# Kernel tuning notes

Hardware: AMD Instinct MI355X
Metric: run time of the kernel (lower is better)

## Reference

```python
import jax, jax.numpy as jnp
import numpy as np

N = 100000   # nodes
E = 400000   # edges
IN = 256
OUT = 256
R = 200      # num relations
B = 32       # num bases


def setup_inputs() -> dict:
    key = jax.random.key(0)
    ks = jax.random.split(key, 7)
    in_feat = jax.random.normal(ks[0], (N, IN), jnp.float32)
    src = jax.random.randint(ks[1], (E,), 0, N, dtype=jnp.int32)
    dst = jax.random.randint(ks[2], (E,), 0, N, dtype=jnp.int32)
    etype = jax.random.randint(ks[3], (E,), 0, R, dtype=jnp.int32)
    # learned params (xavier-ish scale)
    basis = jax.random.normal(ks[4], (B, IN * OUT), jnp.float32) * 0.01
    coef = jax.random.normal(ks[5], (R, B), jnp.float32) * 0.1
    self_loop_weight = jax.random.normal(ks[6], (IN, OUT), jnp.float32) * 0.05
    return {"in_feat": in_feat, "basis": basis, "coef": coef,
            "self_loop_weight": self_loop_weight,
            "src": src, "dst": dst, "etype": etype}


def _rgcn_forward(in_feat, basis, coef, self_loop_weight, src, dst, etype):
    # W_r = reshape(coef @ basis) -> [R, IN, OUT]; msg_e = h_src[e] @ W[etype[e]].
    # Equivalently msg_e = sum_b coef[etype[e], b] * (h_src[e] @ basis_b),
    # computed as B large GEMMs (scan over bases) instead of E tiny bmms,
    # avoiding the [E, IN, OUT] per-edge weight gather.
    basis3 = basis.reshape(B, IN, OUT)          # [B, IN, OUT]
    src_h = in_feat[src]                        # [E, IN]
    c = coef[etype]                             # [E, B]

    def body(acc, xs):
        w_b, c_b = xs                           # [IN, OUT], [E]
        return acc + (src_h @ w_b) * c_b[:, None], None

    msg0 = jnp.zeros((E, OUT), in_feat.dtype)
    msg, _ = jax.lax.scan(body, msg0, (basis3, c.T))   # [E, OUT]

    # mean aggregation over destination nodes (dgl fn.mean)
    agg = jax.ops.segment_sum(msg, dst, num_segments=N)            # [N, OUT]
    deg = jax.ops.segment_sum(jnp.ones((E,), in_feat.dtype), dst, num_segments=N)
    out = agg / jnp.maximum(deg, 1.0)[:, None]  # zero-in-degree nodes -> 0

    # self-loop (bias=False, activation=None, dropout eval no-op)
    out = out + in_feat @ self_loop_weight
    return out


def reference(in_feat, basis, coef, self_loop_weight, src, dst, etype):
    return _rgcn_forward(in_feat, basis, coef, self_loop_weight, src, dst, etype)
```

## Files before the change

### kernel.cpp

```cpp
#include <hip/hip_runtime.h>
#include <hip/hip_bf16.h>


#define NN 100000
#define EE 400000
#define RR 200
#define BB 32
#define MAXTILES 6464
#define EQ2 (MAXTILES * 2 / 8)
#define SCHUNK 2048
#define NSCAN ((NN + 255) / 256)

typedef __attribute__((ext_vector_type(8))) short short8v;
typedef __attribute__((ext_vector_type(4))) float f32x4;

__device__ __forceinline__ unsigned short f2bf(float f) {
  unsigned u = __float_as_uint(f);
  u += 0x7FFF + ((u >> 16) & 1);
  return (unsigned short)(u >> 16);
}
__device__ __forceinline__ float bf2f(unsigned short h) {
  return __uint_as_float(((unsigned)h) << 16);
}

template <bool FEAT>
__global__ __launch_bounds__(256) void k_prep1(
    const float* __restrict__ basis, const float* __restrict__ coef,
    const float* __restrict__ slw, const int* __restrict__ etype,
    const int* __restrict__ dst, const float* __restrict__ in_feat,
    short* __restrict__ wpk, short* __restrict__ spk,
    int* __restrict__ hist, int* __restrict__ deg,
    unsigned short* __restrict__ featb) {
  __shared__ int lh[RR];
  int b = blockIdx.x, tid = threadIdx.x;
  if (b < 800) {
    int ord = (b & 7) * 100 + (b >> 3);
    int rg = ord % 25;
    int pk8 = (ord / 25) * 256 + tid;
    int lane = pk8 & 63;
    int kt = (pk8 >> 6) & 7;
    int ct = pk8 >> 9;
    int n  = ct * 16 + (lane & 15);
    int k0 = kt * 32 + ((lane >> 4) << 3);
    float acc[8][8];
#pragma unroll
    for (int r = 0; r < 8; ++r)
#pragma unroll
      for (int j = 0; j < 8; ++j) acc[r][j] = 0.f;
    for (int bb = 0; bb < BB; ++bb) {
      float bas[8];
#pragma unroll
      for (int j = 0; j < 8; ++j) bas[j] = basis[bb * 65536 + (k0 + j) * 256 + n];
#pragma unroll
      for (int r = 0; r < 8; ++r) {
        float c = coef[(rg * 8 + r) * BB + bb];
#pragma unroll
        for (int j = 0; j < 8; ++j) acc[r][j] += c * bas[j];
      }
    }
#pragma unroll
    for (int r = 0; r < 8; ++r) {
      short8v v;
#pragma unroll
      for (int j = 0; j < 8; ++j) v[j] = (short)f2bf(acc[r][j]);
      *(short8v*)(wpk + (size_t)(rg * 8 + r) * 65536 + (size_t)pk8 * 8) = v;
    }
    return;
  }
  if (b < 832) {
    int t = (b - 800) * 256 + tid;
    int lane = t & 63;
    int kt = (t >> 6) & 7;
    int ct = t >> 9;
    int n  = ct * 16 + (lane & 15);
    int k0 = kt * 32 + ((lane >> 4) << 3);
    short8v v;
#pragma unroll
    for (int j = 0; j < 8; ++j) v[j] = (short)f2bf(slw[(k0 + j) * 256 + n]);
    *(short8v*)(spk + (size_t)t * 8) = v;
    return;
  }
  int hb = b - 832;
  for (int i = tid; i < RR; i += 256) lh[i] = 0;
  __syncthreads();
  for (int e = hb * 256 + tid; e < EE; e += 512 * 256) {
    atomicAdd(&lh[etype[e]], 1);
    atomicAdd(&deg[dst[e]], 1);
  }
  if (FEAT) {
    const int total = NN * 64;
    for (int i = hb * 256 + tid; i < total; i += 512 * 256) {
      float4 v = ((const float4*)in_feat)[i];
      ushort4 h;
      h.x = f2bf(v.x); h.y = f2bf(v.y); h.z = f2bf(v.z); h.w = f2bf(v.w);
      ((ushort4*)featb)[i] = h;
    }
  }
  __syncthreads();
  for (int i = tid; i < RR; i += 256)
    if (lh[i]) atomicAdd(&hist[i], lh[i]);
}

__global__ __launch_bounds__(256) void k_prep2(const int* __restrict__ hist,
                                               const int* __restrict__ deg,
                                               int* __restrict__ cur,
                                               int4* __restrict__ tdesc,
                                               int* __restrict__ bsum) {
  __shared__ int h[RR];
  __shared__ int off[RR];
  __shared__ int toff[RR];
  __shared__ int tot;
  __shared__ int ws4[4];
  int b = blockIdx.x, tid = threadIdx.x;
  if (b == 0) {
    for (int i = tid; i < RR; i += 256) h[i] = hist[i];
    __syncthreads();
    if (tid == 0) {
      int s = 0, ts = 0;
      for (int r = 0; r < RR; ++r) {
        off[r] = s; s += h[r];
        toff[r] = ts; ts += (h[r] + 63) >> 6;
      }
      tot = ts;
    }
    __syncthreads();
    if (tid < RR) {
      int r = tid, cnt = h[r], base = off[r], to = toff[r];
      cur[r] = base;
      int nt = (cnt + 63) >> 6;
      for (int t2 = 0; t2 < nt; ++t2)
        tdesc[to + t2] = make_int4(r, base + t2 * 64, min(64, cnt - t2 * 64), 0);
    }
    for (int i = tot + tid; i < MAXTILES; i += 256)
      tdesc[i] = make_int4(0, 0, 0, 0);
    return;
  }
  int i = (b - 1) * 256 + tid;
  int v = (i < NN) ? deg[i] : 0;
#pragma unroll
  for (int d = 32; d; d >>= 1) v += __shfl_down(v, d, 64);
  if ((tid & 63) == 0) ws4[tid >> 6] = v;
  __syncthreads();
  if (tid == 0) bsum[b - 1] = ws4[0] + ws4[1] + ws4[2] + ws4[3];
}

__global__ __launch_bounds__(256) void k_prep3(const int* __restrict__ deg,
                                               const int* __restrict__ bsum,
                                               int* __restrict__ row_ptr,
                                               int* __restrict__ cur2) {
  __shared__ int ws4[4];
  __shared__ int wo4[4];
  __shared__ int psum[4];
  int tid = threadIdx.x, b = blockIdx.x;
  int sp = 0;
  for (int i = tid; i < b; i += 256) sp += bsum[i];
#pragma unroll
  for (int d = 32; d; d >>= 1) sp += __shfl_down(sp, d, 64);
  if ((tid & 63) == 0) psum[tid >> 6] = sp;
  int i = b * 256 + tid;
  int v = (i < NN) ? deg[i] : 0;
  int x = v;
#pragma unroll
  for (int d = 1; d < 64; d <<= 1) {
    int y = __shfl_up(x, d, 64);
    if ((tid & 63) >= d) x += y;
  }
  if ((tid & 63) == 63) ws4[tid >> 6] = x;
  __syncthreads();
  if (tid == 0) {
    int s = 0;
    for (int w2 = 0; w2 < 4; ++w2) { wo4[w2] = s; s += ws4[w2]; }
    psum[0] = psum[0] + psum[1] + psum[2] + psum[3];
  }
  __syncthreads();
  int excl = x - v + wo4[tid >> 6] + psum[0];
  if (i < NN) { row_ptr[i] = excl; cur2[i] = excl; }
  if (i == 0 && b == 0) row_ptr[NN] = EE;
}

template <bool DL>
__global__ __launch_bounds__(256) void k_prep4(const int* __restrict__ etype,
                                               const int* __restrict__ src,
                                               const int* __restrict__ dst,
                                               const int* __restrict__ deg,
                                               int* __restrict__ cur,
                                               int* __restrict__ gsrc,
                                               int* __restrict__ gdst,
                                               float* __restrict__ ginv,
                                               int* __restrict__ cur2,
                                               int* __restrict__ gout) {
  __shared__ int lh[RR];
  __shared__ int lbase[RR];
  __shared__ int lcur[RR];
  int tid = threadIdx.x;
  int e0 = blockIdx.x * SCHUNK;
  for (int i = tid; i < RR; i += 256) lh[i] = 0;
  __syncthreads();
  for (int i = tid; i < SCHUNK; i += 256) {
    int e = e0 + i;
    if (e < EE) atomicAdd(&lh[etype[e]], 1);
  }
  __syncthreads();
  for (int i = tid; i < RR; i += 256) {
    int c = lh[i];
    lbase[i] = c ? atomicAdd(&cur[i], c) : 0;
    lcur[i] = 0;
  }
  __syncthreads();
  for (int i = tid; i < SCHUNK; i += 256) {
    int e = e0 + i;
    if (e < EE) {
      int et = etype[e];
      int s = lbase[et] + atomicAdd(&lcur[et], 1);
      int d = dst[e];
      gsrc[s] = src[e];
      gdst[s] = d;
      ginv[s] = 1.0f / (float)max(deg[d], 1);
      if (DL) {
        int pos = atomicAdd(&cur2[d], 1);
        gout[s] = pos;
      }
    }
  }
}

__global__ __launch_bounds__(256) void k_edge5(
    const unsigned short* __restrict__ featb, const short* __restrict__ wpk,
    const int* __restrict__ gsrc, const float* __restrict__ ginv,
    const int* __restrict__ gout, const int4* __restrict__ tdesc,
    unsigned short* __restrict__ msg) {
  __shared__ __align__(16) char lA[32768];
  __shared__ int lsrc[64];
  __shared__ float linv[64];
  __shared__ int lout[64];
  int tid = threadIdx.x, wave = tid >> 6, lane = tid & 63;
  int l15 = lane & 15, lg = lane >> 4;
  int bid = blockIdx.x;
  int ord = (bid & 7) * EQ2 + (bid >> 3);
  int tile = ord >> 1, half = ord & 1;
  int4 d = tdesc[tile];
  int rows = d.z;
  if (rows <= 0) return;
  int r = d.x, rs = d.y;
  if (tid < 64) {
    int s = min(rs + tid, EE - 1);
    lsrc[tid] = gsrc[s];
    linv[tid] = ginv[s];
    lout[tid] = gout[s];
  }
  __syncthreads();
  short8v sv[8];
#pragma unroll
  for (int u = 0; u < 8; ++u) {
    int idx = u * 256 + tid;
    int row = idx >> 5, q = idx & 31;
    sv[u] = *(const short8v*)(featb + (size_t)lsrc[row] * 256 + q * 8);
  }
#pragma unroll
  for (int u = 0; u < 8; ++u) {
    int idx = u * 256 + tid;
    int row = idx >> 5, q = idx & 31;
    *(short8v*)(lA + ((row * 512 + q * 16) ^ ((row & 7) << 4))) = sv[u];
  }
  __syncthreads();
  f32x4 acc[4][2];
#pragma unroll
  for (int m = 0; m < 4; ++m)
#pragma unroll
    for (int c = 0; c < 2; ++c) acc[m][c] = (f32x4){0.f, 0.f, 0.f, 0.f};
  const short* bp = wpk + (size_t)r * 65536 +
                    (size_t)(half * 8 + wave * 2) * 4096 + (size_t)lane * 8;
  short8v b0 = *(const short8v*)(bp);
  short8v b1 = *(const short8v*)(bp + 4096);
#pragma unroll
  for (int kt = 0; kt < 8; ++kt) {
    short8v bn0, bn1;
    if (kt < 7) {
      bn0 = *(const short8v*)(bp + (kt + 1) * 512);
      bn1 = *(const short8v*)(bp + 4096 + (kt + 1) * 512);
    }
    short8v a[4];
#pragma unroll
    for (int m = 0; m < 4; ++m) {
      int row = m * 16 + l15;
      a[m] = *(const short8v*)(lA + ((row * 512 + kt * 64 + lg * 16) ^ ((row & 7) << 4)));
    }
#pragma unroll
    for (int m = 0; m < 4; ++m) {
      acc[m][0] = __builtin_amdgcn_mfma_f32_16x16x32_bf16(a[m], b0, acc[m][0], 0, 0, 0);
      acc[m][1] = __builtin_amdgcn_mfma_f32_16x16x32_bf16(a[m], b1, acc[m][1], 0, 0, 0);
    }
    if (kt < 7) { b0 = bn0; b1 = bn1; }
  }
  __syncthreads();
#pragma unroll
  for (int m = 0; m < 4; ++m)
#pragma unroll
    for (int j = 0; j < 4; ++j) {
      int row = m * 16 + lg * 4 + j;
      float inv = linv[row];
      int rb = row * 512, sw = (row & 7) << 4;
#pragma unroll
      for (int c = 0; c < 2; ++c) {
        int col = wave * 32 + c * 16 + l15;
        *(unsigned short*)(lA + ((rb + col * 2) ^ sw)) = f2bf(acc[m][c][j] * inv);
      }
    }
  __syncthreads();
#pragma unroll
  for (int u = 0; u < 4; ++u) {
    int idx = u * 256 + tid;
    int row = idx >> 4, q = idx & 15;
    if (row < rows) {
      short8v vv = *(const short8v*)(lA + ((row * 512 + q * 16) ^ ((row & 7) << 4)));
      *(short8v*)(msg + (size_t)lout[row] * 256 + half * 128 + q * 8) = vv;
    }
  }
}

__global__ __launch_bounds__(256) void k_selfA(const unsigned short* __restrict__ featb,
                                               const short* __restrict__ spk,
                                               float* __restrict__ out) {
  __shared__ __align__(16) char lA[32768];
  int tid = threadIdx.x, wave = tid >> 6, lane = tid & 63;
  int l15 = lane & 15, lg = lane >> 4;
  int n0 = blockIdx.x * 64;
  short8v sv[8];
#pragma unroll
  for (int u = 0; u < 8; ++u) {
    int idx = u * 256 + tid;
    int row = idx >> 5, q = idx & 31;
    int n = min(n0 + row, NN - 1);
    sv[u] = *(const short8v*)(featb + (size_t)n * 256 + q * 8);
  }
#pragma unroll
  for (int u = 0; u < 8; ++u) {
    int idx = u * 256 + tid;
    int row = idx >> 5, q = idx & 31;
    *(short8v*)(lA + ((row * 512 + q * 16) ^ ((row & 7) << 4))) = sv[u];
  }
  __syncthreads();
  f32x4 acc[4][4];
#pragma unroll
  for (int m = 0; m < 4; ++m)
#pragma unroll
    for (int c = 0; c < 4; ++c) acc[m][c] = (f32x4){0.f, 0.f, 0.f, 0.f};
  const short* bp = spk + (size_t)wave * 4 * 4096 + (size_t)lane * 8;
#pragma unroll
  for (int kt = 0; kt < 8; ++kt) {
    short8v a[4], b[4];
#pragma unroll
    for (int c = 0; c < 4; ++c) b[c] = *(const short8v*)(bp + c * 4096 + kt * 512);
#pragma unroll
    for (int m = 0; m < 4; ++m) {
      int row = m * 16 + l15;
      a[m] = *(const short8v*)(lA + ((row * 512 + kt * 64 + lg * 16) ^ ((row & 7) << 4)));
    }
#pragma unroll
    for (int m = 0; m < 4; ++m)
#pragma unroll
      for (int c = 0; c < 4; ++c)
        acc[m][c] = __builtin_amdgcn_mfma_f32_16x16x32_bf16(a[m], b[c], acc[m][c], 0, 0, 0);
  }
#pragma unroll
  for (int m = 0; m < 4; ++m)
#pragma unroll
    for (int j = 0; j < 4; ++j) {
      int n = n0 + m * 16 + lg * 4 + j;
      if (n < NN) {
        float* op = out + (size_t)n * 256 + wave * 64 + l15;
#pragma unroll
        for (int c = 0; c < 4; ++c) op[c * 16] = acc[m][c][j];
      }
    }
}

__global__ __launch_bounds__(256) void k_aggregate(
    const unsigned short* __restrict__ msg, const int* __restrict__ row_ptr,
    float* __restrict__ out) {
  int g = blockIdx.x * 8 + (threadIdx.x >> 5);
  if (g >= NN) return;
  int hl = threadIdx.x & 31;
  int lo = row_ptr[g], hi = row_ptr[g + 1];
  if (lo >= hi) return;
  float a[8];
#pragma unroll
  for (int k = 0; k < 8; ++k) a[k] = 0.f;
  for (int p = lo; p < hi; ++p) {
    short8v mv = *(const short8v*)(msg + (size_t)p * 256 + hl * 8);
#pragma unroll
    for (int k = 0; k < 8; ++k) a[k] += bf2f((unsigned short)mv[k]);
  }
  float* op = out + (size_t)g * 256 + hl * 8;
#pragma unroll
  for (int c = 0; c < 2; ++c) {
    f32x4 o = *(const f32x4*)(op + c * 4);
    o[0] += a[c * 4]; o[1] += a[c * 4 + 1]; o[2] += a[c * 4 + 2]; o[3] += a[c * 4 + 3];
    *(f32x4*)(op + c * 4) = o;
  }
}

__device__ __forceinline__ void gemm64(const char* lA, const short* __restrict__ wpk,
                                       f32x4 acc[4][4], int wave, int lane) {
  int l15 = lane & 15, lg = lane >> 4;
  const short* bp = wpk + (size_t)wave * 4 * 4096 + (size_t)lane * 8;
#pragma unroll
  for (int kt = 0; kt < 8; ++kt) {
    short8v a[4], b[4];
#pragma unroll
    for (int c = 0; c < 4; ++c) b[c] = *(const short8v*)(bp + c * 4096 + kt * 512);
#pragma unroll
    for (int m = 0; m < 4; ++m) {
      int row = m * 16 + l15;
      a[m] = *(const short8v*)(lA + ((row * 512 + kt * 64 + lg * 16) ^ ((row & 7) << 4)));
    }
#pragma unroll
    for (int m = 0; m < 4; ++m)
#pragma unroll
      for (int c = 0; c < 4; ++c)
        acc[m][c] = __builtin_amdgcn_mfma_f32_16x16x32_bf16(a[m], b[c], acc[m][c], 0, 0, 0);
  }
}

template <bool B16>
__global__ __launch_bounds__(256) void k_self_gemm(const float* __restrict__ in_feat,
                                                   const unsigned short* __restrict__ featb,
                                                   const short* __restrict__ spk,
                                                   float* __restrict__ out) {
  __shared__ __align__(16) char lA[32768];
  int n0 = blockIdx.x * 64;
  int tid = threadIdx.x;
  if (B16) {
    short8v sv[8];
#pragma unroll
    for (int u = 0; u < 8; ++u) {
      int idx = u * 256 + tid;
      int row = idx >> 5, q = idx & 31;
      int n = min(n0 + row, NN - 1);
      sv[u] = *(const short8v*)(featb + (size_t)n * 256 + q * 8);
    }
#pragma unroll
    for (int u = 0; u < 8; ++u) {
      int idx = u * 256 + tid;
      int row = idx >> 5, q = idx & 31;
      *(short8v*)(lA + ((row * 512 + q * 16) ^ ((row & 7) << 4))) = sv[u];
    }
  } else {
#pragma unroll
    for (int half = 0; half < 2; ++half) {
      float4 v[8];
#pragma unroll
      for (int u = 0; u < 8; ++u) {
        int it = half * 2048 + u * 256 + tid;
        int row = it >> 6, q = it & 63;
        int n = n0 + row;
        v[u] = (n < NN) ? ((const float4*)(in_feat + (size_t)n * 256))[q]
                        : make_float4(0.f, 0.f, 0.f, 0.f);
      }
#pragma unroll
      for (int u = 0; u < 8; ++u) {
        int it = half * 2048 + u * 256 + tid;
        int row = it >> 6, q = it & 63;
        ushort4 hh;
        hh.x = f2bf(v[u].x); hh.y = f2bf(v[u].y); hh.z = f2bf(v[u].z); hh.w = f2bf(v[u].w);
        *(ushort4*)(lA + ((row * 512 + q * 8) ^ ((row & 7) << 4))) = hh;
      }
    }
  }
  __syncthreads();
  f32x4 acc[4][4];
#pragma unroll
  for (int m = 0; m < 4; ++m)
#pragma unroll
    for (int c = 0; c < 4; ++c) acc[m][c] = (f32x4){0.f, 0.f, 0.f, 0.f};
  int wave = tid >> 6, lane = tid & 63;
  gemm64(lA, spk, acc, wave, lane);
  int l15 = lane & 15, lg = lane >> 4;
#pragma unroll
  for (int m = 0; m < 4; ++m)
#pragma unroll
    for (int j = 0; j < 4; ++j) {
      int n = n0 + m * 16 + lg * 4 + j;
      if (n < NN) {
        float* op = out + (size_t)n * 256 + wave * 64 + l15;
#pragma unroll
        for (int c = 0; c < 4; ++c) op[c * 16] = acc[m][c][j];
      }
    }
}

template <int MODE>
__global__ __launch_bounds__(256) void k_edge_gemmBC(const float* __restrict__ in_feat,
                                                     const unsigned short* __restrict__ featb,
                                                     const short* __restrict__ wpk,
                                                     const int* __restrict__ gsrc,
                                                     const int* __restrict__ gdst,
                                                     const float* __restrict__ ginv,
                                                     const int4* __restrict__ tdesc,
                                                     float* __restrict__ out) {
  __shared__ __align__(16) char lA[32768];
  __shared__ int lsrc[64];
  __shared__ int ldst[64];
  __shared__ float linv[64];
  int bid = blockIdx.x;
  int tile = (bid & 7) * (MAXTILES / 8) + (bid >> 3);
  int4 d = tdesc[tile];
  int rows = d.z;
  if (rows <= 0) return;
  int r = d.x, rs = d.y;
  int tid = threadIdx.x;
  if (tid < 64) {
    if (tid < rows) {
      lsrc[tid] = gsrc[rs + tid];
      ldst[tid] = gdst[rs + tid];
      linv[tid] = ginv[rs + tid];
    } else {
      lsrc[tid] = -1; ldst[tid] = -1; linv[tid] = 0.f;
    }
  }
  __syncthreads();
  if (MODE == 1) {
    short8v sv[8];
#pragma unroll
    for (int u = 0; u < 8; ++u) {
      int idx = u * 256 + tid;
      int row = idx >> 5, q = idx & 31;
      int s = lsrc[row];
      sv[u] = (s >= 0) ? *(const short8v*)(featb + (size_t)s * 256 + q * 8)
                       : (short8v){0, 0, 0, 0, 0, 0, 0, 0};
    }
#pragma unroll
    for (int u = 0; u < 8; ++u) {
      int idx = u * 256 + tid;
      int row = idx >> 5, q = idx & 31;
      *(short8v*)(lA + ((row * 512 + q * 16) ^ ((row & 7) << 4))) = sv[u];
    }
  } else {
#pragma unroll
    for (int half = 0; half < 2; ++half) {
      float4 v[8];
#pragma unroll
      for (int u = 0; u < 8; ++u) {
        int it = half * 2048 + u * 256 + tid;
        int row = it >> 6, q = it & 63;
        int s = lsrc[row];
        v[u] = (s >= 0) ? ((const float4*)(in_feat + (size_t)s * 256))[q]
                        : make_float4(0.f, 0.f, 0.f, 0.f);
      }
#pragma unroll
      for (int u = 0; u < 8; ++u) {
        int it = half * 2048 + u * 256 + tid;
        int row = it >> 6, q = it & 63;
        ushort4 hh;
        hh.x = f2bf(v[u].x); hh.y = f2bf(v[u].y); hh.z = f2bf(v[u].z); hh.w = f2bf(v[u].w);
        *(ushort4*)(lA + ((row * 512 + q * 8) ^ ((row & 7) << 4))) = hh;
      }
    }
  }
  __syncthreads();
  f32x4 acc[4][4];
#pragma unroll
  for (int m = 0; m < 4; ++m)
#pragma unroll
    for (int c = 0; c < 4; ++c) acc[m][c] = (f32x4){0.f, 0.f, 0.f, 0.f};
  int wave = tid >> 6, lane = tid & 63;
  gemm64(lA, wpk + (size_t)r * 65536, acc, wave, lane);
  int l15 = lane & 15, lg = lane >> 4;
#pragma unroll
  for (int m = 0; m < 4; ++m)
#pragma unroll
    for (int j = 0; j < 4; ++j) {
      int row = m * 16 + lg * 4 + j;
      int dd = ldst[row];
      if (dd >= 0) {
        float inv = linv[row];
        float* op = out + (size_t)dd * 256 + wave * 64 + l15;
#pragma unroll
        for (int c = 0; c < 4; ++c) unsafeAtomicAdd(op + c * 16, acc[m][c][j] * inv);
      }
    }
}

extern "C" void kernel_launch(void* const* d_in, const int* in_sizes, int n_in,
                              void* d_out, int out_size, void* d_ws, size_t ws_size,
                              hipStream_t stream) {
  const float* in_feat = (const float*)d_in[0];
  const float* basis   = (const float*)d_in[1];
  const float* coef    = (const float*)d_in[2];
  const float* slw     = (const float*)d_in[3];
  const int*   src     = (const int*)d_in[4];
  const int*   dst     = (const int*)d_in[5];
  const int*   etype   = (const int*)d_in[6];
  float* out = (float*)d_out;

  char* base = (char*)d_ws;
  char* w = base;
  auto alloc = [&](size_t bytes) {
    char* p = w;
    w += (bytes + 255) & ~(size_t)255;
    return p;
  };
  short* wpk  = (short*)alloc((size_t)RR * 65536 * 2);
  short* spk  = (short*)alloc(65536 * 2);
  int*   gsrc = (int*)alloc((size_t)EE * 4);
  int*   gdst = (int*)alloc((size_t)EE * 4);
  float* ginv = (float*)alloc((size_t)EE * 4);
  int*   deg  = (int*)alloc((size_t)NN * 4);
  int*   hist = (int*)alloc(RR * 4);
  int*   cur  = (int*)alloc(RR * 4);
  int4*  tdesc = (int4*)alloc((size_t)MAXTILES * 16);
  int*   bsum = (int*)alloc(NSCAN * 4);
  unsigned short* featb = (unsigned short*)alloc((size_t)NN * 256 * 2);
  size_t need_b = (size_t)(w - base);
  int* row_ptr = (int*)alloc((size_t)(NN + 1) * 4);
  int* cur2    = (int*)alloc((size_t)NN * 4);
  int* gout    = (int*)alloc((size_t)EE * 4);
  unsigned short* msg = (unsigned short*)alloc((size_t)EE * 256 * 2);
  size_t need_a = (size_t)(w - base);

  bool tierA = ws_size >= need_a;
  bool tierB = ws_size >= need_b;

  hipMemsetAsync(hist, 0, RR * 4, stream);
  hipMemsetAsync(deg, 0, (size_t)NN * 4, stream);

  if (tierA) {
    k_prep1<true><<<1344, 256, 0, stream>>>(basis, coef, slw, etype, dst, in_feat,
                                            wpk, spk, hist, deg, featb);
    k_prep2<<<NSCAN + 1, 256, 0, stream>>>(hist, deg, cur, tdesc, bsum);
    k_prep3<<<NSCAN, 256, 0, stream>>>(deg, bsum, row_ptr, cur2);
    k_prep4<true><<<(EE + SCHUNK - 1) / SCHUNK, 256, 0, stream>>>(
        etype, src, dst, deg, cur, gsrc, gdst, ginv, cur2, gout);
    k_selfA<<<(NN + 63) / 64, 256, 0, stream>>>(featb, spk, out);
    k_edge5<<<MAXTILES * 2, 256, 0, stream>>>(featb, wpk, gsrc, ginv, gout,
                                              tdesc, msg);
    k_aggregate<<<(NN + 7) / 8, 256, 0, stream>>>(msg, row_ptr, out);
  } else if (tierB) {
    k_prep1<true><<<1344, 256, 0, stream>>>(basis, coef, slw, etype, dst, in_feat,
                                            wpk, spk, hist, deg, featb);
    k_prep2<<<NSCAN + 1, 256, 0, stream>>>(hist, deg, cur, tdesc, bsum);
    k_prep4<false><<<(EE + SCHUNK - 1) / SCHUNK, 256, 0, stream>>>(
        etype, src, dst, deg, cur, gsrc, gdst, ginv, nullptr, nullptr);
    k_self_gemm<true><<<(NN + 63) / 64, 256, 0, stream>>>(in_feat, featb, spk, out);
    k_edge_gemmBC<1><<<MAXTILES, 256, 0, stream>>>(in_feat, featb, wpk, gsrc, gdst,
                                                   ginv, tdesc, out);
  } else {
    k_prep1<false><<<1344, 256, 0, stream>>>(basis, coef, slw, etype, dst, in_feat,
                                             wpk, spk, hist, deg, nullptr);
    k_prep2<<<NSCAN + 1, 256, 0, stream>>>(hist, deg, cur, tdesc, bsum);
    k_prep4<false><<<(EE + SCHUNK - 1) / SCHUNK, 256, 0, stream>>>(
        etype, src, dst, deg, cur, gsrc, gdst, ginv, nullptr, nullptr);
    k_self_gemm<false><<<(NN + 63) / 64, 256, 0, stream>>>(in_feat, nullptr, spk, out);
    k_edge_gemmBC<0><<<MAXTILES, 256, 0, stream>>>(in_feat, nullptr, wpk, gsrc, gdst,
                                                   ginv, tdesc, out);
  }
}
```

Before: 364.4 us.

## Merge self-loop GEMM into edge GEMM kernel as extra blocks, skip gdst write

Folds the self-loop GEMM kernel into the edge message kernel as additional trailing blocks, each computing half of the output columns to match the edge kernel's tile shape. This removes one launch and lets self-loop and edge work share the GPU instead of running back-to-back. The prep kernel also stops writing gdst in the path that does not use it, saving some global stores. The trade-off is twice as many self-loop blocks, each reloading the same 64-row feature tile, and larger code with branches inside one kernel.

```diff
diff --git a/kernel.cpp b/kernel.cpp
--- a/kernel.cpp
+++ b/kernel.cpp
@@ -8,6 +8,8 @@
 #define BB 32
 #define MAXTILES 6464
 #define EQ2 (MAXTILES * 2 / 8)
+#define EGRID2 (MAXTILES * 2)
+#define SGRID (((NN + 63) / 64) * 2)
 #define SCHUNK 2048
 #define NSCAN ((NN + 255) / 256)
 
@@ -214,21 +216,23 @@
       int s = lbase[et] + atomicAdd(&lcur[et], 1);
       int d = dst[e];
       gsrc[s] = src[e];
-      gdst[s] = d;
       ginv[s] = 1.0f / (float)max(deg[d], 1);
       if (DL) {
         int pos = atomicAdd(&cur2[d], 1);
         gout[s] = pos;
-      }
-    }
-  }
-}
-
-__global__ __launch_bounds__(256) void k_edge5(
+      } else {
+        gdst[s] = d;
+      }
+    }
+  }
+}
+
+__global__ __launch_bounds__(256) void k_main(
     const unsigned short* __restrict__ featb, const short* __restrict__ wpk,
-    const int* __restrict__ gsrc, const float* __restrict__ ginv,
-    const int* __restrict__ gout, const int4* __restrict__ tdesc,
-    unsigned short* __restrict__ msg) {
+    const short* __restrict__ spk, const int* __restrict__ gsrc,
+    const float* __restrict__ ginv, const int* __restrict__ gout,
+    const int4* __restrict__ tdesc, unsigned short* __restrict__ msg,
+    float* __restrict__ out) {
   __shared__ __align__(16) char lA[32768];
   __shared__ int lsrc[64];
   __shared__ float linv[64];
@@ -236,25 +240,100 @@
   int tid = threadIdx.x, wave = tid >> 6, lane = tid & 63;
   int l15 = lane & 15, lg = lane >> 4;
   int bid = blockIdx.x;
-  int ord = (bid & 7) * EQ2 + (bid >> 3);
-  int tile = ord >> 1, half = ord & 1;
-  int4 d = tdesc[tile];
-  int rows = d.z;
-  if (rows <= 0) return;
-  int r = d.x, rs = d.y;
-  if (tid < 64) {
-    int s = min(rs + tid, EE - 1);
-    lsrc[tid] = gsrc[s];
-    linv[tid] = ginv[s];
-    lout[tid] = gout[s];
-  }
-  __syncthreads();
+
+  if (bid < EGRID2) {
+    int ord = (bid & 7) * EQ2 + (bid >> 3);
+    int tile = ord >> 1, half = ord & 1;
+    int4 d = tdesc[tile];
+    int rows = d.z;
+    if (rows <= 0) return;
+    int r = d.x, rs = d.y;
+    if (tid < 64) {
+      int s = min(rs + tid, EE - 1);
+      lsrc[tid] = gsrc[s];
+      linv[tid] = ginv[s];
+      lout[tid] = gout[s];
+    }
+    __syncthreads();
+    short8v sv[8];
+#pragma unroll
+    for (int u = 0; u < 8; ++u) {
+      int idx = u * 256 + tid;
+      int row = idx >> 5, q = idx & 31;
+      sv[u] = *(const short8v*)(featb + (size_t)lsrc[row] * 256 + q * 8);
+    }
+#pragma unroll
+    for (int u = 0; u < 8; ++u) {
+      int idx = u * 256 + tid;
+      int row = idx >> 5, q = idx & 31;
+      *(short8v*)(lA + ((row * 512 + q * 16) ^ ((row & 7) << 4))) = sv[u];
+    }
+    __syncthreads();
+    f32x4 acc[4][2];
+#pragma unroll
+    for (int m = 0; m < 4; ++m)
+#pragma unroll
+      for (int c = 0; c < 2; ++c) acc[m][c] = (f32x4){0.f, 0.f, 0.f, 0.f};
+    const short* bp = wpk + (size_t)r * 65536 +
+                      (size_t)(half * 8 + wave * 2) * 4096 + (size_t)lane * 8;
+    short8v b0 = *(const short8v*)(bp);
+    short8v b1 = *(const short8v*)(bp + 4096);
+#pragma unroll
+    for (int kt = 0; kt < 8; ++kt) {
+      short8v bn0, bn1;
+      if (kt < 7) {
+        bn0 = *(const short8v*)(bp + (kt + 1) * 512);
+        bn1 = *(const short8v*)(bp + 4096 + (kt + 1) * 512);
+      }
+      short8v a[4];
+#pragma unroll
+      for (int m = 0; m < 4; ++m) {
+        int row = m * 16 + l15;
+        a[m] = *(const short8v*)(lA + ((row * 512 + kt * 64 + lg * 16) ^ ((row & 7) << 4)));
+      }
+#pragma unroll
+      for (int m = 0; m < 4; ++m) {
+        acc[m][0] = __builtin_amdgcn_mfma_f32_16x16x32_bf16(a[m], b0, acc[m][0], 0, 0, 0);
+        acc[m][1] = __builtin_amdgcn_mfma_f32_16x16x32_bf16(a[m], b1, acc[m][1], 0, 0, 0);
+      }
+      if (kt < 7) { b0 = bn0; b1 = bn1; }
+    }
+    __syncthreads();
+#pragma unroll
+    for (int m = 0; m < 4; ++m)
+#pragma unroll
+      for (int j = 0; j < 4; ++j) {
+        int row = m * 16 + lg * 4 + j;
+        float inv = linv[row];
+        int rb = row * 512, sw = (row & 7) << 4;
+#pragma unroll
+        for (int c = 0; c < 2; ++c) {
+          int col = wave * 32 + c * 16 + l15;
+          *(unsigned short*)(lA + ((rb + col * 2) ^ sw)) = f2bf(acc[m][c][j] * inv);
+        }
+      }
+    __syncthreads();
+#pragma unroll
+    for (int u = 0; u < 4; ++u) {
+      int idx = u * 256 + tid;
+      int row = idx >> 4, q = idx & 15;
+      if (row < rows) {
+        short8v vv = *(const short8v*)(lA + ((row * 512 + q * 16) ^ ((row & 7) << 4)));
+        *(short8v*)(msg + (size_t)lout[row] * 256 + half * 128 + q * 8) = vv;
+      }
+    }
+    return;
+  }
+
+  int b2 = bid - EGRID2;
+  int n0 = (b2 >> 1) * 64, half = b2 & 1;
   short8v sv[8];
 #pragma unroll
   for (int u = 0; u < 8; ++u) {
     int idx = u * 256 + tid;
     int row = idx >> 5, q = idx & 31;
-    sv[u] = *(const short8v*)(featb + (size_t)lsrc[row] * 256 + q * 8);
+    int n = min(n0 + row, NN - 1);
+    sv[u] = *(const short8v*)(featb + (size_t)n * 256 + q * 8);
   }
 #pragma unroll
   for (int u = 0; u < 8; ++u) {
@@ -268,8 +347,7 @@
   for (int m = 0; m < 4; ++m)
 #pragma unroll
     for (int c = 0; c < 2; ++c) acc[m][c] = (f32x4){0.f, 0.f, 0.f, 0.f};
-  const short* bp = wpk + (size_t)r * 65536 +
-                    (size_t)(half * 8 + wave * 2) * 4096 + (size_t)lane * 8;
+  const short* bp = spk + (size_t)(half * 8 + wave * 2) * 4096 + (size_t)lane * 8;
   short8v b0 = *(const short8v*)(bp);
   short8v b1 = *(const short8v*)(bp + 4096);
 #pragma unroll
@@ -292,85 +370,15 @@
     }
     if (kt < 7) { b0 = bn0; b1 = bn1; }
   }
-  __syncthreads();
-#pragma unroll
-  for (int m = 0; m < 4; ++m)
-#pragma unroll
-    for (int j = 0; j < 4; ++j) {
-      int row = m * 16 + lg * 4 + j;
-      float inv = linv[row];
-      int rb = row * 512, sw = (row & 7) << 4;
-#pragma unroll
-      for (int c = 0; c < 2; ++c) {
-        int col = wave * 32 + c * 16 + l15;
-        *(unsigned short*)(lA + ((rb + col * 2) ^ sw)) = f2bf(acc[m][c][j] * inv);
-      }
-    }
-  __syncthreads();
-#pragma unroll
-  for (int u = 0; u < 4; ++u) {
-    int idx = u * 256 + tid;
-    int row = idx >> 4, q = idx & 15;
-    if (row < rows) {
-      short8v vv = *(const short8v*)(lA + ((row * 512 + q * 16) ^ ((row & 7) << 4)));
-      *(short8v*)(msg + (size_t)lout[row] * 256 + half * 128 + q * 8) = vv;
-    }
-  }
-}
-
-__global__ __launch_bounds__(256) void k_selfA(const unsigned short* __restrict__ featb,
-                                               const short* __restrict__ spk,
-                                               float* __restrict__ out) {
-  __shared__ __align__(16) char lA[32768];
-  int tid = threadIdx.x, wave = tid >> 6, lane = tid & 63;
-  int l15 = lane & 15, lg = lane >> 4;
-  int n0 = blockIdx.x * 64;
-  short8v sv[8];
-#pragma unroll
-  for (int u = 0; u < 8; ++u) {
-    int idx = u * 256 + tid;
-    int row = idx >> 5, q = idx & 31;
-    int n = min(n0 + row, NN - 1);
-    sv[u] = *(const short8v*)(featb + (size_t)n * 256 + q * 8);
-  }
-#pragma unroll
-  for (int u = 0; u < 8; ++u) {
-    int idx = u * 256 + tid;
-    int row = idx >> 5, q = idx & 31;
-    *(short8v*)(lA + ((row * 512 + q * 16) ^ ((row & 7) << 4))) = sv[u];
-  }
-  __syncthreads();
-  f32x4 acc[4][4];
-#pragma unroll
-  for (int m = 0; m < 4; ++m)
-#pragma unroll
-    for (int c = 0; c < 4; ++c) acc[m][c] = (f32x4){0.f, 0.f, 0.f, 0.f};
-  const short* bp = spk + (size_t)wave * 4 * 4096 + (size_t)lane * 8;
-#pragma unroll
-  for (int kt = 0; kt < 8; ++kt) {
-    short8v a[4], b[4];
-#pragma unroll
-    for (int c = 0; c < 4; ++c) b[c] = *(const short8v*)(bp + c * 4096 + kt * 512);
-#pragma unroll
-    for (int m = 0; m < 4; ++m) {
-      int row = m * 16 + l15;
-      a[m] = *(const short8v*)(lA + ((row * 512 + kt * 64 + lg * 16) ^ ((row & 7) << 4)));
-    }
-#pragma unroll
-    for (int m = 0; m < 4; ++m)
-#pragma unroll
-      for (int c = 0; c < 4; ++c)
-        acc[m][c] = __builtin_amdgcn_mfma_f32_16x16x32_bf16(a[m], b[c], acc[m][c], 0, 0, 0);
-  }
 #pragma unroll
   for (int m = 0; m < 4; ++m)
 #pragma unroll
     for (int j = 0; j < 4; ++j) {
       int n = n0 + m * 16 + lg * 4 + j;
       if (n < NN) {
-        float* op = out + (size_t)n * 256 + wave * 64 + l15;
-#pragma unroll
-        for (int c = 0; c < 4; ++c) op[c * 16] = acc[m][c][j];
+        float* op = out + (size_t)n * 256 + half * 128 + wave * 32 + l15;
+        op[0]  = acc[m][0][j];
+        op[16] = acc[m][1][j];
       }
     }
 }
@@ -631,9 +639,8 @@
     k_prep3<<<NSCAN, 256, 0, stream>>>(deg, bsum, row_ptr, cur2);
     k_prep4<true><<<(EE + SCHUNK - 1) / SCHUNK, 256, 0, stream>>>(
         etype, src, dst, deg, cur, gsrc, gdst, ginv, cur2, gout);
-    k_selfA<<<(NN + 63) / 64, 256, 0, stream>>>(featb, spk, out);
-    k_edge5<<<MAXTILES * 2, 256, 0, stream>>>(featb, wpk, gsrc, ginv, gout,
-                                              tdesc, msg);
+    k_main<<<EGRID2 + SGRID, 256, 0, stream>>>(featb, wpk, spk, gsrc, ginv, gout,
+                                               tdesc, msg, out);
     k_aggregate<<<(NN + 7) / 8, 256, 0, stream>>>(msg, row_ptr, out);
   } else if (tierB) {
     k_prep1<true><<<1344, 256, 0, stream>>>(basis, coef, slw, etype, dst, in_feat,
```

Result: faster. 344.3 us (-5.5%).
